# Kernel tuning notes

Measured on AMD Instinct MI355X. Metric: run time of the kernel, lower is better.

The kernel has to match this reference:

```python
import jax, jax.numpy as jnp
import numpy as np

B, T, D = 2, 2048, 1024
H, DH, CTX = 16, 64, 2048
EPS = 1e-6

def setup_inputs() -> dict:
    key = jax.random.key(0)
    ks = jax.random.split(key, 8)
    s = lambda d: 1.0 / np.sqrt(d)
    return {
        'x':       jax.random.normal(ks[0], (B, T, D), jnp.float32),
        'w_norm1': jnp.ones((D,), jnp.float32),
        'w_qkv':   jax.random.normal(ks[1], (3 * D, D), jnp.float32) * s(D),
        'w_proj':  jax.random.normal(ks[2], (D, D), jnp.float32) * s(D),
        'w_norm2': jnp.ones((D,), jnp.float32),
        'w_gate':  jax.random.normal(ks[3], (4 * D, D), jnp.float32) * s(D),
        'w_up':    jax.random.normal(ks[4], (4 * D, D), jnp.float32) * s(D),
        'w_down':  jax.random.normal(ks[5], (D, 4 * D), jnp.float32) * s(4 * D),
        'step':    0,
    }

def _rmsnorm(x, w):
    return x * jax.lax.rsqrt(jnp.mean(x * x, axis=-1, keepdims=True) + EPS) * w

def reference(x, w_norm1, w_qkv, w_proj, w_norm2, w_gate, w_up, w_down, step):
    # Prefill path (kv_cache is None, step == 0): full causal attention over T tokens.
    b, t, d = x.shape
    scale = 1.0 / np.sqrt(DH)
    h = _rmsnorm(x, w_norm1)
    qkv = (h @ w_qkv.T).reshape(b, t, 3, H, DH).transpose(2, 0, 3, 1, 4)  # [3,B,H,T,Dh]
    q, k, v = qkv[0], qkv[1], qkv[2]
    att = jnp.einsum('bhqd,bhkd->bhqk', q, k) * scale           # [B,H,T,T]
    causal = jnp.tril(jnp.ones((t, t), bool))
    att = jnp.where(causal, att, jnp.float32(-jnp.inf))
    att = jax.nn.softmax(att, axis=-1)
    out = jnp.einsum('bhqk,bhkd->bhqd', att, v)                 # [B,H,T,Dh]
    out = out.transpose(0, 2, 1, 3).reshape(b, t, d)
    x = x + out @ w_proj.T
    h2 = _rmsnorm(x, w_norm2)
    x = x + (jax.nn.silu(h2 @ w_gate.T) * (h2 @ w_up.T)) @ w_down.T
    # Append-only KV cache, zero-padded to ctx length as in the torch module.
    k_cache = jnp.zeros((b, H, CTX, DH), x.dtype).at[:, :, :t].set(k)
    v_cache = jnp.zeros((b, H, CTX, DH), x.dtype).at[:, :, :t].set(v)
    return (x, k_cache, v_cache)
```

## Files before the change

kernel.cpp:

```cpp
#include <hip/hip_runtime.h>
#include <hip/hip_bf16.h>
#include <cstdint>
#include <cstddef>


using bf16x8 = __attribute__((ext_vector_type(8))) __bf16;
using f32x4  = __attribute__((ext_vector_type(4))) float;

#define VMCNT(n) asm volatile("s_waitcnt vmcnt(" #n ")" ::: "memory")
#define LGKM0()  do { asm volatile("s_waitcnt lgkmcnt(0)" ::: "memory"); \
                      __builtin_amdgcn_sched_barrier(0); } while (0)
#define BARF()   do { asm volatile("" ::: "memory"); __builtin_amdgcn_s_barrier(); \
                      asm volatile("" ::: "memory"); } while (0)

__device__ __forceinline__ short f2b(float f) {
  uint32_t u = __builtin_bit_cast(uint32_t, f);
  uint32_t r = (u + 0x7FFFu + ((u >> 16) & 1u)) >> 16;
  return (short)r;
}
__device__ __forceinline__ float b2f(short s) {
  uint32_t u = ((uint32_t)(uint16_t)s) << 16;
  return __builtin_bit_cast(float, u);
}
__device__ __forceinline__ uint32_t pack2(float a, float b) {
  return (__builtin_bit_cast(uint32_t, a) >> 16) |
         (__builtin_bit_cast(uint32_t, b) & 0xFFFF0000u);
}

__device__ __forceinline__ void gload16(const short* g, short* l) {
  __builtin_amdgcn_global_load_lds(
      (const __attribute__((address_space(1))) void*)g,
      (__attribute__((address_space(3))) void*)l, 16, 0, 0);
}

template<int ROWS>
__device__ __forceinline__ void stage_swz(const short* __restrict__ g, int ldg,
                                          short* lds, int tid) {
#pragma unroll
  for (int jj = 0; jj < ROWS / 32; ++jj) {
    int row = jj * 32 + (tid >> 3);
    int seg = tid & 7;
    gload16(g + (size_t)row * ldg + ((seg ^ (row & 7)) << 3),
            lds + row * 64 + (seg << 3));
  }
}

__device__ __forceinline__ void stage_round512(const short* __restrict__ g, int ldg,
                                               short* lds, int tid, int rbase) {
  int row = rbase + (tid >> 3);
  int seg = tid & 7;
  gload16(g + (size_t)row * ldg + ((seg ^ (row & 7)) << 3),
          lds + row * 64 + (seg << 3));
}

__device__ __forceinline__ bf16x8 frag64(const short* lds, int row, int seg) {
  return *(const bf16x8*)(lds + row * 64 + ((seg ^ (row & 7)) << 3));
}

__device__ __forceinline__ f32x4 mma16(bf16x8 a, bf16x8 b, f32x4 c) {
  return __builtin_amdgcn_mfma_f32_16x16x32_bf16(a, b, c, 0, 0, 0);
}

__global__ void k_cvt_all(const float* __restrict__ wqkv, short* __restrict__ oqkv,
                          const float* __restrict__ wproj, short* __restrict__ oproj,
                          const float* __restrict__ wgate, short* __restrict__ ogate,
                          const float* __restrict__ wup, short* __restrict__ oup,
                          const float* __restrict__ wdown, short* __restrict__ odown) {
  int bid = blockIdx.x;
  const float* src;
  short* dst;
  int off;
  if (bid < 3072)       { src = wqkv;  dst = oqkv;  off = bid; }
  else if (bid < 4096)  { src = wproj; dst = oproj; off = bid - 3072; }
  else if (bid < 8192)  { src = wgate; dst = ogate; off = bid - 4096; }
  else if (bid < 12288) { src = wup;   dst = oup;   off = bid - 8192; }
  else                  { src = wdown; dst = odown; off = bid - 12288; }
  int i = off * 256 + threadIdx.x;
  float4 v = ((const float4*)src)[i];
  ((short4*)dst)[i] = make_short4(f2b(v.x), f2b(v.y), f2b(v.z), f2b(v.w));
}

__global__ void k_rms(const float* __restrict__ x, const float* __restrict__ w,
                      short* __restrict__ out) {
  int row = blockIdx.x;
  int tid = threadIdx.x;
  float4 v = *(const float4*)(x + (size_t)row * 1024 + tid * 4);
  float ss = v.x * v.x + v.y * v.y + v.z * v.z + v.w * v.w;
#pragma unroll
  for (int o = 1; o < 64; o <<= 1) ss += __shfl_xor(ss, o);
  __shared__ float sred[4];
  int wid = tid >> 6, lane = tid & 63;
  if (lane == 0) sred[wid] = ss;
  __syncthreads();
  float tot = sred[0] + sred[1] + sred[2] + sred[3];
  float r = rsqrtf(tot * (1.0f / 1024.0f) + 1e-6f);
  float4 wv = *(const float4*)(w + tid * 4);
  short4 o = make_short4(f2b(v.x * r * wv.x), f2b(v.y * r * wv.y),
                         f2b(v.z * r * wv.z), f2b(v.w * r * wv.w));
  *(short4*)(out + (size_t)row * 1024 + tid * 4) = o;
}

__global__ __launch_bounds__(512) void k_qkv(
    const short* __restrict__ A, const short* __restrict__ W,
    short* __restrict__ q_b, short* __restrict__ k_b, short* __restrict__ vT_b,
    float* __restrict__ kc, float* __restrict__ vc) {
  const int K = 1024, nk = 16;
  __shared__ short As[2][128 * 64];
  __shared__ short Bq[2][128 * 64];
  __shared__ short Bk[2][128 * 64];
  __shared__ short Bv[2][128 * 64];
  int tid = threadIdx.x;
  int bid = blockIdx.x;
  int swz = (bid & 7) * 32 + (bid >> 3);
  int bx = swz & 7, by = swz >> 3;
  int m0 = by * 128, n0 = bx * 128;
  int w = tid >> 6, l = tid & 63;
  int wr = w >> 2, wc = w & 3;
  int lr = l & 15, lseg = l >> 4;
  f32x4 aq[4][2] = {}, ak[4][2] = {}, av[4][2] = {};
  const short* Ab = A + (size_t)m0 * K;
  const short* Qb = W + (size_t)n0 * K;
  const short* Kb = W + (size_t)(1024 + n0) * K;
  const short* Vb = W + (size_t)(2048 + n0) * K;

  stage_round512(Ab, K, &As[0][0], tid, 0);
  stage_round512(Ab, K, &As[0][0], tid, 64);
  stage_round512(Qb, K, &Bq[0][0], tid, 0);
  stage_round512(Qb, K, &Bq[0][0], tid, 64);
  stage_round512(Kb, K, &Bk[0][0], tid, 0);
  stage_round512(Kb, K, &Bk[0][0], tid, 64);
  stage_round512(Vb, K, &Bv[0][0], tid, 0);
  stage_round512(Vb, K, &Bv[0][0], tid, 64);
  stage_round512(Ab + 64, K, &As[1][0], tid, 0);
  stage_round512(Ab + 64, K, &As[1][0], tid, 64);

  bf16x8 a[4][2], b[2][2];
#pragma unroll 2
  for (int t = 0; t < nk; ++t) {
    short* Sa = &As[t & 1][0];
    short* Sq = &Bq[t & 1][0];
    short* Sk = &Bk[t & 1][0];
    short* Sv = &Bv[t & 1][0];
    short* SqN = &Bq[(t + 1) & 1][0];
    short* SkN = &Bk[(t + 1) & 1][0];
    short* SvN = &Bv[(t + 1) & 1][0];
    const short* Ag2 = Ab + (size_t)(t + 2) * 64;
    const short* Qg1 = Qb + (size_t)(t + 1) * 64;
    const short* Kg1 = Kb + (size_t)(t + 1) * 64;
    const short* Vg1 = Vb + (size_t)(t + 1) * 64;
    bool pf1 = (t + 1 < nk), pf2 = (t + 2 < nk);

    VMCNT(2);
    BARF();

#pragma unroll
    for (int i = 0; i < 4; ++i)
#pragma unroll
      for (int kk = 0; kk < 2; ++kk)
        a[i][kk] = frag64(Sa, wr * 64 + i * 16 + lr, kk * 4 + lseg);
#pragma unroll
    for (int j = 0; j < 2; ++j)
#pragma unroll
      for (int kk = 0; kk < 2; ++kk)
        b[j][kk] = frag64(Sq, wc * 32 + j * 16 + lr, kk * 4 + lseg);
    if (pf1) {
      stage_round512(Qg1, K, SqN, tid, 0);
      stage_round512(Qg1, K, SqN, tid, 64);
      stage_round512(Kg1, K, SkN, tid, 0);
      stage_round512(Kg1, K, SkN, tid, 64);
    }
    BARF();
    LGKM0();
    __builtin_amdgcn_s_setprio(1);
#pragma unroll
    for (int i = 0; i < 4; ++i)
#pragma unroll
      for (int j = 0; j < 2; ++j) {
        aq[i][j] = mma16(a[i][0], b[j][0], aq[i][j]);
        aq[i][j] = mma16(a[i][1], b[j][1], aq[i][j]);
      }
    __builtin_amdgcn_s_setprio(0);

#pragma unroll
    for (int j = 0; j < 2; ++j)
#pragma unroll
      for (int kk = 0; kk < 2; ++kk)
        b[j][kk] = frag64(Sk, wc * 32 + j * 16 + lr, kk * 4 + lseg);
    if (pf1) {
      stage_round512(Vg1, K, SvN, tid, 0);
      stage_round512(Vg1, K, SvN, tid, 64);
    }
    BARF();
    LGKM0();
    __builtin_amdgcn_s_setprio(1);
#pragma unroll
    for (int i = 0; i < 4; ++i)
#pragma unroll
      for (int j = 0; j < 2; ++j) {
        ak[i][j] = mma16(a[i][0], b[j][0], ak[i][j]);
        ak[i][j] = mma16(a[i][1], b[j][1], ak[i][j]);
      }
    __builtin_amdgcn_s_setprio(0);

#pragma unroll
    for (int j = 0; j < 2; ++j)
#pragma unroll
      for (int kk = 0; kk < 2; ++kk)
        b[j][kk] = frag64(Sv, wc * 32 + j * 16 + lr, kk * 4 + lseg);
    if (pf2) {
      stage_round512(Ag2, K, Sa, tid, 0);
      stage_round512(Ag2, K, Sa, tid, 64);
    }
    BARF();
    LGKM0();
    __builtin_amdgcn_s_setprio(1);
#pragma unroll
    for (int i = 0; i < 4; ++i)
#pragma unroll
      for (int j = 0; j < 2; ++j) {
        av[i][j] = mma16(a[i][0], b[j][0], av[i][j]);
        av[i][j] = mma16(a[i][1], b[j][1], av[i][j]);
      }
    __builtin_amdgcn_s_setprio(0);
  }

#pragma unroll
  for (int i = 0; i < 4; ++i) {
#pragma unroll
    for (int j = 0; j < 2; ++j) {
#pragma unroll
      for (int r = 0; r < 4; ++r) {
        int m = m0 + wr * 64 + i * 16 + lseg * 4 + r;
        int n = n0 + wc * 32 + j * 16 + lr;
        int hh = n >> 6, dh = n & 63;
        int b_ = m >> 11, tt = m & 2047;
        int bh = b_ * 16 + hh;
        size_t idx = ((size_t)bh * 2048 + tt) * 64 + dh;
        q_b[idx] = f2b(aq[i][j][r]);
        float fk = ak[i][j][r];
        k_b[idx] = f2b(fk);
        kc[idx] = fk;
        float fv = av[i][j][r];
        vT_b[((size_t)bh * 64 + dh) * 2048 + tt] = f2b(fv);
        vc[idx] = fv;
      }
    }
  }
}

__global__ __launch_bounds__(512) void k_mlp(
    const short* __restrict__ A, const short* __restrict__ Wg,
    const short* __restrict__ Wu, short* __restrict__ outb) {
  const int K = 1024, N = 4096, nk = 16;
  __shared__ short As[2][256 * 64];
  __shared__ short Bg[2][128 * 64];
  __shared__ short Bu[2][128 * 64];
  int tid = threadIdx.x;
  int bid = blockIdx.x;
  int xcd = bid & 7, idx = bid >> 3;
  int bx = xcd * 4 + (idx & 3);
  int by = idx >> 2;
  int m0 = by * 256, n0 = bx * 128;
  int w = tid >> 6, l = tid & 63;
  int wr = w >> 2, wc = w & 3;
  int lr = l & 15, lseg = l >> 4;
  f32x4 aG[2][4][2] = {}, aU[2][4][2] = {};
  const short* Ab = A + (size_t)m0 * K;
  const short* Gb = Wg + (size_t)n0 * K;
  const short* Ub = Wu + (size_t)n0 * K;

  stage_round512(Ab, K, &As[0][0], tid, 0);
  stage_round512(Ab, K, &As[0][0], tid, 64);
  stage_round512(Ab, K, &As[0][0], tid, 128);
  stage_round512(Ab, K, &As[0][0], tid, 192);
  stage_round512(Gb, K, &Bg[0][0], tid, 0);
  stage_round512(Gb, K, &Bg[0][0], tid, 64);
  stage_round512(Ub, K, &Bu[0][0], tid, 0);
  stage_round512(Ub, K, &Bu[0][0], tid, 64);
  stage_round512(Ab + 64, K, &As[1][0], tid, 0);
  stage_round512(Ab + 64, K, &As[1][0], tid, 64);
  stage_round512(Ab + 64, K, &As[1][0], tid, 128);
  stage_round512(Ab + 64, K, &As[1][0], tid, 192);

  bf16x8 a0[4][2], a1[4][2], bg[2][2], bu[2][2];
#pragma unroll 2
  for (int t = 0; t < nk; ++t) {
    short* Sa  = &As[t & 1][0];
    short* Sg  = &Bg[t & 1][0];
    short* Su  = &Bu[t & 1][0];
    short* SgN = &Bg[(t + 1) & 1][0];
    short* SuN = &Bu[(t + 1) & 1][0];
    const short* Ag2 = Ab + (size_t)(t + 2) * 64;
    const short* Gg1 = Gb + (size_t)(t + 1) * 64;
    const short* Ug1 = Ub + (size_t)(t + 1) * 64;
    bool pf1 = (t + 1 < nk), pf2 = (t + 2 < nk);

    VMCNT(4);
    BARF();

#pragma unroll
    for (int i = 0; i < 4; ++i)
#pragma unroll
      for (int kk = 0; kk < 2; ++kk)
        a0[i][kk] = frag64(Sa, wr * 128 + i * 16 + lr, kk * 4 + lseg);
#pragma unroll
    for (int j = 0; j < 2; ++j)
#pragma unroll
      for (int kk = 0; kk < 2; ++kk)
        bg[j][kk] = frag64(Sg, wc * 32 + j * 16 + lr, kk * 4 + lseg);
    if (pf1) {
      stage_round512(Gg1, K, SgN, tid, 0);
      stage_round512(Gg1, K, SgN, tid, 64);
      stage_round512(Ug1, K, SuN, tid, 0);
      stage_round512(Ug1, K, SuN, tid, 64);
    }
    BARF();
    LGKM0();
    __builtin_amdgcn_s_setprio(1);
#pragma unroll
    for (int i = 0; i < 4; ++i)
#pragma unroll
      for (int j = 0; j < 2; ++j) {
        aG[0][i][j] = mma16(a0[i][0], bg[j][0], aG[0][i][j]);
        aG[0][i][j] = mma16(a0[i][1], bg[j][1], aG[0][i][j]);
      }
    __builtin_amdgcn_s_setprio(0);

#pragma unroll
    for (int j = 0; j < 2; ++j)
#pragma unroll
      for (int kk = 0; kk < 2; ++kk)
        bu[j][kk] = frag64(Su, wc * 32 + j * 16 + lr, kk * 4 + lseg);
    if (pf2) {
      stage_round512(Ag2, K, Sa, tid, 0);
      stage_round512(Ag2, K, Sa, tid, 128);
    }
    BARF();
    LGKM0();
    __builtin_amdgcn_s_setprio(1);
#pragma unroll
    for (int i = 0; i < 4; ++i)
#pragma unroll
      for (int j = 0; j < 2; ++j) {
        aU[0][i][j] = mma16(a0[i][0], bu[j][0], aU[0][i][j]);
        aU[0][i][j] = mma16(a0[i][1], bu[j][1], aU[0][i][j]);
      }
    __builtin_amdgcn_s_setprio(0);

#pragma unroll
    for (int i = 0; i < 4; ++i)
#pragma unroll
      for (int kk = 0; kk < 2; ++kk)
        a1[i][kk] = frag64(Sa, wr * 128 + 64 + i * 16 + lr, kk * 4 + lseg);
    BARF();
    LGKM0();
    __builtin_amdgcn_s_setprio(1);
#pragma unroll
    for (int i = 0; i < 4; ++i)
#pragma unroll
      for (int j = 0; j < 2; ++j) {
        aG[1][i][j] = mma16(a1[i][0], bg[j][0], aG[1][i][j]);
        aG[1][i][j] = mma16(a1[i][1], bg[j][1], aG[1][i][j]);
      }
    __builtin_amdgcn_s_setprio(0);

    if (pf2) {
      stage_round512(Ag2, K, Sa, tid, 64);
      stage_round512(Ag2, K, Sa, tid, 192);
    }
    BARF();
    __builtin_amdgcn_s_setprio(1);
#pragma unroll
    for (int i = 0; i < 4; ++i)
#pragma unroll
      for (int j = 0; j < 2; ++j) {
        aU[1][i][j] = mma16(a1[i][0], bu[j][0], aU[1][i][j]);
        aU[1][i][j] = mma16(a1[i][1], bu[j][1], aU[1][i][j]);
      }
    __builtin_amdgcn_s_setprio(0);
  }

#pragma unroll
  for (int qm = 0; qm < 2; ++qm) {
#pragma unroll
    for (int i = 0; i < 4; ++i) {
#pragma unroll
      for (int j = 0; j < 2; ++j) {
#pragma unroll
        for (int r = 0; r < 4; ++r) {
          int m = m0 + wr * 128 + qm * 64 + i * 16 + lseg * 4 + r;
          int n = n0 + wc * 32 + j * 16 + lr;
          float g = aG[qm][i][j][r];
          float u = aU[qm][i][j][r];
          float s = g / (1.0f + __expf(-g));
          outb[(size_t)m * N + n] = f2b(s * u);
        }
      }
    }
  }
}

__global__ __launch_bounds__(512) void k_down(
    const short* __restrict__ A, const short* __restrict__ Bw,
    short* __restrict__ pc0, short* __restrict__ pc1) {
  const int K = 4096, nk = 32;
  __shared__ short As[2][256 * 64];
  __shared__ short Bs[2][128 * 64];
  int tid = threadIdx.x;
  int bid = blockIdx.x;
  int xcd = bid & 7, idx = bid >> 3;
  int ks = idx & 1;
  int by = idx >> 1;
  int bx = xcd;
  int m0 = by * 256, n0 = bx * 128;
  int w = tid >> 6, l = tid & 63;
  int wr = w >> 2, wc = w & 3;
  int lr = l & 15, lseg = l >> 4;
  f32x4 acc[2][4][2] = {};
  const short* Ab = A + (size_t)m0 * K + ks * 2048;
  const short* Bb = Bw + (size_t)n0 * K + ks * 2048;
  short* pc = ks ? pc1 : pc0;

  stage_round512(Ab, K, &As[0][0], tid, 0);
  stage_round512(Ab, K, &As[0][0], tid, 64);
  stage_round512(Ab, K, &As[0][0], tid, 128);
  stage_round512(Ab, K, &As[0][0], tid, 192);
  stage_round512(Bb, K, &Bs[0][0], tid, 0);
  stage_round512(Bb, K, &Bs[0][0], tid, 64);
  stage_round512(Ab + 64, K, &As[1][0], tid, 0);
  stage_round512(Ab + 64, K, &As[1][0], tid, 128);
  stage_round512(Bb + 64, K, &Bs[1][0], tid, 0);
  stage_round512(Bb + 64, K, &Bs[1][0], tid, 64);

  bf16x8 a0[4][2], a1[4][2], b[2][2];
#pragma unroll 2
  for (int t = 0; t < nk; ++t) {
    int s = t & 1;
    short* Sa = &As[s][0];
    short* Sb = &Bs[s][0];
    short* SaN = &As[s ^ 1][0];
    const short* Ag1 = Ab + (size_t)(t + 1) * 64;
    const short* Ag2 = Ab + (size_t)(t + 2) * 64;
    const short* Bg2 = Bb + (size_t)(t + 2) * 64;
    bool pf1 = (t + 1 < nk), pf2 = (t + 2 < nk);

    VMCNT(4);
    BARF();

#pragma unroll
    for (int i = 0; i < 4; ++i)
#pragma unroll
      for (int kk = 0; kk < 2; ++kk)
        a0[i][kk] = frag64(Sa, wr * 128 + i * 16 + lr, kk * 4 + lseg);
#pragma unroll
    for (int j = 0; j < 2; ++j)
#pragma unroll
      for (int kk = 0; kk < 2; ++kk)
        b[j][kk] = frag64(Sb, wc * 32 + j * 16 + lr, kk * 4 + lseg);
    if (pf1) {
      stage_round512(Ag1, K, SaN, tid, 64);
      stage_round512(Ag1, K, SaN, tid, 192);
    }
    BARF();
    LGKM0();
    __builtin_amdgcn_s_setprio(1);
#pragma unroll
    for (int i = 0; i < 4; ++i)
#pragma unroll
      for (int j = 0; j < 2; ++j) {
        acc[0][i][j] = mma16(a0[i][0], b[j][0], acc[0][i][j]);
        acc[0][i][j] = mma16(a0[i][1], b[j][1], acc[0][i][j]);
      }
    __builtin_amdgcn_s_setprio(0);

#pragma unroll
    for (int i = 0; i < 4; ++i)
#pragma unroll
      for (int kk = 0; kk < 2; ++kk)
        a1[i][kk] = frag64(Sa, wr * 128 + 64 + i * 16 + lr, kk * 4 + lseg);
    BARF();
    if (pf2) {
      stage_round512(Ag2, K, Sa, tid, 0);
      stage_round512(Ag2, K, Sa, tid, 128);
      stage_round512(Bg2, K, Sb, tid, 0);
      stage_round512(Bg2, K, Sb, tid, 64);
    }
    LGKM0();
    __builtin_amdgcn_s_setprio(1);
#pragma unroll
    for (int i = 0; i < 4; ++i)
#pragma unroll
      for (int j = 0; j < 2; ++j) {
        acc[1][i][j] = mma16(a1[i][0], b[j][0], acc[1][i][j]);
        acc[1][i][j] = mma16(a1[i][1], b[j][1], acc[1][i][j]);
      }
    __builtin_amdgcn_s_setprio(0);
  }

#pragma unroll
  for (int qm = 0; qm < 2; ++qm) {
#pragma unroll
    for (int i = 0; i < 4; ++i) {
#pragma unroll
      for (int j = 0; j < 2; ++j) {
#pragma unroll
        for (int r = 0; r < 4; ++r) {
          int m = m0 + wr * 128 + qm * 64 + i * 16 + lseg * 4 + r;
          int n = n0 + wc * 32 + j * 16 + lr;
          pc[(size_t)m * 1024 + n] = f2b(acc[qm][i][j][r]);
        }
      }
    }
  }
}

__global__ void k_fin(float* __restrict__ out, const short* __restrict__ pc0,
                      const short* __restrict__ pc1) {
  int i = blockIdx.x * 256 + threadIdx.x;
  float4 v = ((const float4*)out)[i];
  short4 p0 = ((const short4*)pc0)[i];
  short4 p1 = ((const short4*)pc1)[i];
  v.x += b2f(p0.x) + b2f(p1.x);
  v.y += b2f(p0.y) + b2f(p1.y);
  v.z += b2f(p0.z) + b2f(p1.z);
  v.w += b2f(p0.w) + b2f(p1.w);
  ((float4*)out)[i] = v;
}

__global__ __launch_bounds__(256, 2) void k_gemm_skinny(
    const short* __restrict__ A, const short* __restrict__ Bw,
    int M, int N, int K, int gx,
    const float* __restrict__ res, float* __restrict__ outf) {
  __shared__ short As[3][128 * 64];
  __shared__ short Bs[3][64 * 64];
  int tid = threadIdx.x;
  int nwg = gridDim.x, bid = blockIdx.x;
  int swz = (bid & 7) * (nwg >> 3) + (bid >> 3);
  int bx = swz % gx, by = swz / gx;
  int m0 = by * 128, n0 = bx * 64;
  int w = tid >> 6, l = tid & 63;
  int wr = w >> 1, wc = w & 1;
  int lr = l & 15, lseg = l >> 4;
  f32x4 acc[4][2] = {};
  int nk = K >> 6;
  const short* Ab = A + (size_t)m0 * K;
  const short* Bb = Bw + (size_t)n0 * K;

  stage_swz<128>(Ab, K, &As[0][0], tid);
  stage_swz<64>(Bb, K, &Bs[0][0], tid);
  stage_swz<128>(Ab + 64, K, &As[1][0], tid);
  stage_swz<64>(Bb + 64, K, &Bs[1][0], tid);

#pragma unroll 1
  for (int u = 0; u < nk; ++u) {
    VMCNT(6);
    BARF();
    if (u + 2 < nk) {
      int sl = (u + 2) % 3;
      stage_swz<128>(Ab + (u + 2) * 64, K, &As[sl][0], tid);
      stage_swz<64>(Bb + (u + 2) * 64, K, &Bs[sl][0], tid);
    }
    const short* Asl = &As[u % 3][0];
    const short* Bsl = &Bs[u % 3][0];
    bf16x8 ar[4][2], br[2][2];
#pragma unroll
    for (int i = 0; i < 4; ++i)
#pragma unroll
      for (int kk = 0; kk < 2; ++kk)
        ar[i][kk] = frag64(Asl, wr * 64 + i * 16 + lr, kk * 4 + lseg);
#pragma unroll
    for (int j = 0; j < 2; ++j)
#pragma unroll
      for (int kk = 0; kk < 2; ++kk)
        br[j][kk] = frag64(Bsl, wc * 32 + j * 16 + lr, kk * 4 + lseg);
    LGKM0();
    __builtin_amdgcn_s_setprio(1);
#pragma unroll
    for (int i = 0; i < 4; ++i)
#pragma unroll
      for (int j = 0; j < 2; ++j) {
        acc[i][j] = mma16(ar[i][0], br[j][0], acc[i][j]);
        acc[i][j] = mma16(ar[i][1], br[j][1], acc[i][j]);
      }
    __builtin_amdgcn_s_setprio(0);
  }

#pragma unroll
  for (int i = 0; i < 4; ++i) {
#pragma unroll
    for (int j = 0; j < 2; ++j) {
#pragma unroll
      for (int r = 0; r < 4; ++r) {
        int m = m0 + wr * 64 + i * 16 + (l >> 4) * 4 + r;
        int n = n0 + wc * 32 + j * 16 + lr;
        outf[(size_t)m * N + n] = acc[i][j][r] + res[(size_t)m * N + n];
      }
    }
  }
}

template<int NC>
__device__ __forceinline__ void attn_tile(
    const short* __restrict__ Ksl, const short* __restrict__ Vsl,
    short* __restrict__ pw,
    const bf16x8 (&qf)[2][2], f32x4 (&acc)[2][4],
    float (&mrow)[2], float (&dden)[2],
    int kv0, int qb0, int qb1, bool band0, bool band1,
    int lr, int g) {
  bf16x8 kf[4][2], vb[2][4];
#pragma unroll
  for (int i = 0; i < 4; ++i)
#pragma unroll
    for (int kk = 0; kk < 2; ++kk)
      kf[i][kk] = frag64(Ksl, i * 16 + lr, kk * 4 + g);
#pragma unroll
  for (int kk = 0; kk < 2; ++kk)
#pragma unroll
    for (int jf = 0; jf < 4; ++jf)
      vb[kk][jf] = frag64(Vsl, jf * 16 + lr, kk * 4 + g);

  f32x4 st[NC][4];
#pragma unroll
  for (int c = 0; c < NC; ++c) {
    int cc = (NC == 2) ? c : 1;
#pragma unroll
    for (int i = 0; i < 4; ++i) {
      f32x4 z = {};
      z = mma16(kf[i][0], qf[cc][0], z);
      z = mma16(kf[i][1], qf[cc][1], z);
      st[c][i] = z;
    }
  }

  const float SC = 0.125f * 1.44269504f;
  float p[NC][16], pm[NC], corr[NC];
#pragma unroll
  for (int c = 0; c < NC; ++c) {
    int cc = (NC == 2) ? c : 1;
    bool band = (cc == 0) ? band0 : band1;
    int qgc = ((cc == 0) ? qb0 : qb1) + lr;
    float m_ = -INFINITY;
#pragma unroll
    for (int i = 0; i < 4; ++i)
#pragma unroll
      for (int r = 0; r < 4; ++r) {
        float v = st[c][i][r] * SC;
        if (band) {
          int key = kv0 + i * 16 + g * 4 + r;
          if (key > qgc) v = -INFINITY;
        }
        p[c][i * 4 + r] = v;
        m_ = fmaxf(m_, v);
      }
    pm[c] = m_;
  }
#pragma unroll
  for (int c = 0; c < NC; ++c) pm[c] = fmaxf(pm[c], __shfl_xor(pm[c], 16));
#pragma unroll
  for (int c = 0; c < NC; ++c) pm[c] = fmaxf(pm[c], __shfl_xor(pm[c], 32));
  float dsum[NC];
#pragma unroll
  for (int c = 0; c < NC; ++c) {
    int cc = (NC == 2) ? c : 1;
    float nm = fmaxf(mrow[cc], pm[c]);
    corr[c] = exp2f(mrow[cc] - nm);
    mrow[cc] = nm;
    float ds_ = 0.0f;
#pragma unroll
    for (int kx = 0; kx < 16; ++kx) {
      float pv = exp2f(p[c][kx] - nm);
      p[c][kx] = pv;
      ds_ += pv;
    }
    dsum[c] = ds_;
  }
#pragma unroll
  for (int c = 0; c < NC; ++c) dsum[c] += __shfl_xor(dsum[c], 16);
#pragma unroll
  for (int c = 0; c < NC; ++c) dsum[c] += __shfl_xor(dsum[c], 32);
#pragma unroll
  for (int c = 0; c < NC; ++c) {
    int cc = (NC == 2) ? c : 1;
    dden[cc] = dden[cc] * corr[c] + dsum[c];
  }

#pragma unroll
  for (int c = 0; c < NC; ++c) {
    int cc = (NC == 2) ? c : 1;
#pragma unroll
    for (int r = 0; r < 4; ++r) {
      float cr = __shfl(corr[c], g * 4 + r);
#pragma unroll
      for (int jf = 0; jf < 4; ++jf) acc[cc][jf][r] *= cr;
    }
    int prow = cc * 16 + lr;
#pragma unroll
    for (int i = 0; i < 4; ++i) {
      uint2 pk;
      pk.x = pack2(p[c][i * 4 + 0], p[c][i * 4 + 1]);
      pk.y = pack2(p[c][i * 4 + 2], p[c][i * 4 + 3]);
      int seg = (i * 2 + (g >> 1)) ^ (prow & 7);
      *(uint2*)(pw + prow * 64 + seg * 8 + (g & 1) * 4) = pk;
    }
  }

#pragma unroll
  for (int c = 0; c < NC; ++c) {
    int cc = (NC == 2) ? c : 1;
    int prow = cc * 16 + lr;
#pragma unroll
    for (int kk = 0; kk < 2; ++kk) {
      bf16x8 pa = *(const bf16x8*)(pw + prow * 64 + (((kk * 4 + g) ^ (prow & 7)) << 3));
#pragma unroll
      for (int jf = 0; jf < 4; ++jf)
        acc[cc][jf] = mma16(pa, vb[kk][jf], acc[cc][jf]);
    }
  }
}

__global__ __launch_bounds__(256, 2) void k_attn(const short* __restrict__ q_b,
                                                 const short* __restrict__ k_b,
                                                 const short* __restrict__ vT_b,
                                                 short* __restrict__ o_b) {
  __shared__ short Ks[3][64 * 64];
  __shared__ short VTs[3][64 * 64];
  __shared__ short Ps[4][32 * 64];
  int tid = threadIdx.x;
  int w = tid >> 6, l = tid & 63;
  int lr = l & 15, g = l >> 4;
  int ib = blockIdx.x, bh = blockIdx.y;
  int qlo = ib, qhi = 31 - ib;
  int qb0 = qlo * 64 + w * 16;
  int qb1 = qhi * 64 + w * 16;

  bf16x8 qf[2][2];
  const short* Qg = q_b + (size_t)bh * 2048 * 64;
#pragma unroll
  for (int kk = 0; kk < 2; ++kk) {
    qf[0][kk] = *(const bf16x8*)(Qg + (size_t)(qb0 + lr) * 64 + kk * 32 + g * 8);
    qf[1][kk] = *(const bf16x8*)(Qg + (size_t)(qb1 + lr) * 64 + kk * 32 + g * 8);
  }

  f32x4 acc[2][4] = {};
  float mrow[2] = {-INFINITY, -INFINITY};
  float dden[2] = {0.0f, 0.0f};
  int nt = qhi + 1;
  const short* Kg = k_b + (size_t)bh * 2048 * 64;
  const short* Vg = vT_b + (size_t)bh * 64 * 2048;
  short* pw = &Ps[w][0];

  stage_swz<64>(Kg, 64, &Ks[0][0], tid);
  stage_swz<64>(Vg, 2048, &VTs[0][0], tid);
  stage_swz<64>(Kg + 64 * 64, 64, &Ks[1][0], tid);
  stage_swz<64>(Vg + 64, 2048, &VTs[1][0], tid);

#pragma unroll 1
  for (int kt = 0; kt <= qlo; ++kt) {
    VMCNT(4);
    BARF();
    if (kt + 2 < nt) {
      int sl = (kt + 2) % 3;
      stage_swz<64>(Kg + (size_t)(kt + 2) * 64 * 64, 64, &Ks[sl][0], tid);
      stage_swz<64>(Vg + (kt + 2) * 64, 2048, &VTs[sl][0], tid);
    }
    int s = kt % 3;
    attn_tile<2>(&Ks[s][0], &VTs[s][0], pw, qf, acc, mrow, dden,
                 kt * 64, qb0, qb1, kt == qlo, false, lr, g);
  }
#pragma unroll 1
  for (int kt = qlo + 1; kt < nt; ++kt) {
    VMCNT(4);
    BARF();
    if (kt + 2 < nt) {
      int sl = (kt + 2) % 3;
      stage_swz<64>(Kg + (size_t)(kt + 2) * 64 * 64, 64, &Ks[sl][0], tid);
      stage_swz<64>(Vg + (kt + 2) * 64, 2048, &VTs[sl][0], tid);
    }
    int s = kt % 3;
    attn_tile<1>(&Ks[s][0], &VTs[s][0], pw, qf, acc, mrow, dden,
                 kt * 64, qb0, qb1, false, kt == qhi, lr, g);
  }

  int hh = bh & 15, b_ = bh >> 4;
#pragma unroll
  for (int c = 0; c < 2; ++c) {
    int qbc = (c == 0) ? qb0 : qb1;
#pragma unroll
    for (int r = 0; r < 4; ++r) {
      float dq = __shfl(dden[c], g * 4 + r);
      float inv = 1.0f / dq;
      int mg = qbc + g * 4 + r;
      size_t rowoff = ((size_t)b_ * 2048 + mg) * 1024 + hh * 64;
#pragma unroll
      for (int jf = 0; jf < 4; ++jf)
        o_b[rowoff + jf * 16 + lr] = f2b(acc[c][jf][r] * inv);
    }
  }
}

extern "C" void kernel_launch(void* const* d_in, const int* in_sizes, int n_in,
                              void* d_out, int out_size, void* d_ws, size_t ws_size,
                              hipStream_t stream) {
  const float* x     = (const float*)d_in[0];
  const float* wn1   = (const float*)d_in[1];
  const float* wqkv  = (const float*)d_in[2];
  const float* wproj = (const float*)d_in[3];
  const float* wn2   = (const float*)d_in[4];
  const float* wgate = (const float*)d_in[5];
  const float* wup   = (const float*)d_in[6];
  const float* wdown = (const float*)d_in[7];
  float* out = (float*)d_out;
  char* ws = (char*)d_ws;

  short* wqkv_b  = (short*)(ws + 0);
  short* wproj_b = (short*)(ws + 6291456);
  short* wgate_b = (short*)(ws + 8388608);
  short* wup_b   = (short*)(ws + 16777216);
  short* wdown_b = (short*)(ws + 25165824);
  short* h_b     = (short*)(ws + 33554432);
  short* q_b     = (short*)(ws + 41943040);
  short* k_b     = (short*)(ws + 50331648);
  short* vT_b    = (short*)(ws + 58720256);
  short* ao_b    = (short*)(ws + 67108864);
  short* act_b   = q_b;
  short* pc0     = wgate_b;
  short* pc1     = wup_b;
  float* x1 = out;
  float* kc = out + 4194304;
  float* vc = out + 8388608;

  k_cvt_all<<<16384, 256, 0, stream>>>(wqkv, wqkv_b, wproj, wproj_b,
                                       wgate, wgate_b, wup, wup_b, wdown, wdown_b);

  k_rms<<<4096, 256, 0, stream>>>(x, wn1, h_b);

  k_qkv<<<256, 512, 0, stream>>>(h_b, wqkv_b, q_b, k_b, vT_b, kc, vc);

  k_attn<<<dim3(16, 32), 256, 0, stream>>>(q_b, k_b, vT_b, ao_b);

  k_gemm_skinny<<<512, 256, 0, stream>>>(ao_b, wproj_b, 4096, 1024, 1024, 16,
                                         x, x1);

  k_rms<<<4096, 256, 0, stream>>>(x1, wn2, h_b);

  k_mlp<<<512, 512, 0, stream>>>(h_b, wgate_b, wup_b, act_b);

  k_down<<<256, 512, 0, stream>>>(act_b, wdown_b, pc0, pc1);
  k_fin<<<4096, 256, 0, stream>>>(out, pc0, pc1);
}
```

Baseline: 270.0 us.

## Restructure gate/up GEMM main loop into two phases with rescheduled A prefetch

The fused gate/up GEMM loop goes from four barrier-separated compute phases per k-step to two. Gate and up B fragments are loaded together and both accumulators are updated in each phase. Half of the A-tile prefetch for step t+1 (rows 64 and 192) is moved into the first phase, and the vmcnt wait changes accordingly. This is meant to cut barrier and LDS-wait overhead per iteration, at the cost of higher register pressure, a different prefetch distance, and correctness that depends on the new wait counts.

```diff
diff --git a/kernel.cpp b/kernel.cpp
--- a/kernel.cpp
+++ b/kernel.cpp
@@ -278,24 +278,25 @@
   stage_round512(Ub, K, &Bu[0][0], tid, 0);
   stage_round512(Ub, K, &Bu[0][0], tid, 64);
   stage_round512(Ab + 64, K, &As[1][0], tid, 0);
-  stage_round512(Ab + 64, K, &As[1][0], tid, 64);
   stage_round512(Ab + 64, K, &As[1][0], tid, 128);
-  stage_round512(Ab + 64, K, &As[1][0], tid, 192);
 
   bf16x8 a0[4][2], a1[4][2], bg[2][2], bu[2][2];
 #pragma unroll 2
   for (int t = 0; t < nk; ++t) {
-    short* Sa  = &As[t & 1][0];
-    short* Sg  = &Bg[t & 1][0];
-    short* Su  = &Bu[t & 1][0];
-    short* SgN = &Bg[(t + 1) & 1][0];
-    short* SuN = &Bu[(t + 1) & 1][0];
+    int s = t & 1;
+    short* Sa  = &As[s][0];
+    short* Sg  = &Bg[s][0];
+    short* Su  = &Bu[s][0];
+    short* SaN = &As[s ^ 1][0];
+    short* SgN = &Bg[s ^ 1][0];
+    short* SuN = &Bu[s ^ 1][0];
+    const short* Ag1 = Ab + (size_t)(t + 1) * 64;
     const short* Ag2 = Ab + (size_t)(t + 2) * 64;
     const short* Gg1 = Gb + (size_t)(t + 1) * 64;
     const short* Ug1 = Ub + (size_t)(t + 1) * 64;
     bool pf1 = (t + 1 < nk), pf2 = (t + 2 < nk);
 
-    VMCNT(4);
+    VMCNT(2);
     BARF();
 
 #pragma unroll
@@ -306,13 +307,17 @@
 #pragma unroll
     for (int j = 0; j < 2; ++j)
 #pragma unroll
-      for (int kk = 0; kk < 2; ++kk)
+      for (int kk = 0; kk < 2; ++kk) {
         bg[j][kk] = frag64(Sg, wc * 32 + j * 16 + lr, kk * 4 + lseg);
+        bu[j][kk] = frag64(Su, wc * 32 + j * 16 + lr, kk * 4 + lseg);
+      }
     if (pf1) {
       stage_round512(Gg1, K, SgN, tid, 0);
       stage_round512(Gg1, K, SgN, tid, 64);
       stage_round512(Ug1, K, SuN, tid, 0);
       stage_round512(Ug1, K, SuN, tid, 64);
+      stage_round512(Ag1, K, SaN, tid, 64);
+      stage_round512(Ag1, K, SaN, tid, 192);
     }
     BARF();
     LGKM0();
@@ -323,14 +328,16 @@
       for (int j = 0; j < 2; ++j) {
         aG[0][i][j] = mma16(a0[i][0], bg[j][0], aG[0][i][j]);
         aG[0][i][j] = mma16(a0[i][1], bg[j][1], aG[0][i][j]);
+        aU[0][i][j] = mma16(a0[i][0], bu[j][0], aU[0][i][j]);
+        aU[0][i][j] = mma16(a0[i][1], bu[j][1], aU[0][i][j]);
       }
     __builtin_amdgcn_s_setprio(0);
 
 #pragma unroll
-    for (int j = 0; j < 2; ++j)
-#pragma unroll
-      for (int kk = 0; kk < 2; ++kk)
-        bu[j][kk] = frag64(Su, wc * 32 + j * 16 + lr, kk * 4 + lseg);
+    for (int i = 0; i < 4; ++i)
+#pragma unroll
+      for (int kk = 0; kk < 2; ++kk)
+        a1[i][kk] = frag64(Sa, wr * 128 + 64 + i * 16 + lr, kk * 4 + lseg);
     if (pf2) {
       stage_round512(Ag2, K, Sa, tid, 0);
       stage_round512(Ag2, K, Sa, tid, 128);
@@ -342,38 +349,8 @@
     for (int i = 0; i < 4; ++i)
 #pragma unroll
       for (int j = 0; j < 2; ++j) {
-        aU[0][i][j] = mma16(a0[i][0], bu[j][0], aU[0][i][j]);
-        aU[0][i][j] = mma16(a0[i][1], bu[j][1], aU[0][i][j]);
-      }
-    __builtin_amdgcn_s_setprio(0);
-
-#pragma unroll
-    for (int i = 0; i < 4; ++i)
-#pragma unroll
-      for (int kk = 0; kk < 2; ++kk)
-        a1[i][kk] = frag64(Sa, wr * 128 + 64 + i * 16 + lr, kk * 4 + lseg);
-    BARF();
-    LGKM0();
-    __builtin_amdgcn_s_setprio(1);
-#pragma unroll
-    for (int i = 0; i < 4; ++i)
-#pragma unroll
-      for (int j = 0; j < 2; ++j) {
         aG[1][i][j] = mma16(a1[i][0], bg[j][0], aG[1][i][j]);
         aG[1][i][j] = mma16(a1[i][1], bg[j][1], aG[1][i][j]);
-      }
-    __builtin_amdgcn_s_setprio(0);
-
-    if (pf2) {
-      stage_round512(Ag2, K, Sa, tid, 64);
-      stage_round512(Ag2, K, Sa, tid, 192);
-    }
-    BARF();
-    __builtin_amdgcn_s_setprio(1);
-#pragma unroll
-    for (int i = 0; i < 4; ++i)
-#pragma unroll
-      for (int j = 0; j < 2; ++j) {
         aU[1][i][j] = mma16(a1[i][0], bu[j][0], aU[1][i][j]);
         aU[1][i][j] = mma16(a1[i][1], bu[j][1], aU[1][i][j]);
       }
```

Result: no change. 266.4 us (-1.3%).
